# Performance work log

Measured on AMD Instinct MI355X. Metric: run time of the kernel, lower is better.

Reference implementation:

```python
import jax, jax.numpy as jnp
import numpy as np


def setup_inputs() -> dict:
    key = jax.random.key(0)
    ks = jax.random.split(key, 5)
    B, S, D, U = 4, 2048, 1024, 1024
    scale = 1.0 / np.sqrt(D)
    return {
        "query": jax.random.normal(ks[0], (B, S, D), dtype=jnp.float32),
        "value": jax.random.normal(ks[1], (B, S, D), dtype=jnp.float32),
        "Wq": jax.random.normal(ks[2], (D, U), dtype=jnp.float32) * scale,
        "bq": jnp.zeros((U,), dtype=jnp.float32),
        "Wk": jax.random.normal(ks[3], (D, U), dtype=jnp.float32) * scale,
        "bk": jnp.zeros((U,), dtype=jnp.float32),
        "Wv": jax.random.normal(ks[4], (D, U), dtype=jnp.float32) * scale,
        "bv": jnp.zeros((U,), dtype=jnp.float32),
    }


def reference(query, value, Wq, bq, Wk, bk, Wv, bv):
    # Dense projections (last-dim matmul + bias)
    Q = jnp.einsum("bsd,du->bsu", query, Wq) + bq   # [B,Sq,U]
    K = jnp.einsum("btd,du->btu", value, Wk) + bk   # [B,Sk,U]
    V = jnp.einsum("btd,du->btu", value, Wv) + bv   # [B,Sk,U]
    d_k = jnp.asarray(K.shape[-1], dtype=jnp.float32)
    scores = jnp.einsum("bsu,btu->bst", Q, K) / jnp.sqrt(d_k)  # [B,Sq,Sk]
    weights = jax.nn.softmax(scores, axis=-1)
    return jnp.einsum("bst,btu->bsu", weights, V)   # [B,Sq,U]
```

## Files before the change

kernel.cpp:

```cpp
#include <hip/hip_runtime.h>
#include <hip/hip_bf16.h>
#include <stdint.h>

#define DEVINL __device__ __forceinline__

typedef __attribute__((ext_vector_type(4))) float f32x4;
typedef __attribute__((ext_vector_type(8))) __bf16 bfv8;
typedef __attribute__((ext_vector_type(8))) short s16x8;
typedef __attribute__((ext_vector_type(4))) short s16x4;

DEVINL short f2bf(float f) {
  union { float f; unsigned u; } v; v.f = f;
  unsigned r = v.u + 0x7FFFu + ((v.u >> 16) & 1u);
  return (short)(r >> 16);
}
DEVINL float bf2f(short h) {
  union { unsigned u; float f; } v; v.u = ((unsigned)(unsigned short)h) << 16;
  return v.f;
}
DEVINL void gload_lds16(const void* g, void* l) {
  __builtin_amdgcn_global_load_lds((__attribute__((address_space(1))) unsigned*)(g),
                                   (__attribute__((address_space(3))) unsigned*)(l),
                                   16, 0, 0);
}
#define S_BARRIER() __builtin_amdgcn_s_barrier()
#define MEMORD() asm volatile("" ::: "memory")
template <int N> DEVINL void vmwaitc() {
  asm volatile("s_waitcnt vmcnt(%0)" :: "i"(N) : "memory");
}
DEVINL int xswz(int p, int n) { return (p & 7) * (n >> 3) + (p >> 3); }

template <int BU, int NF, int RING>
DEVINL void gemm_core(const short* __restrict__ Ag, const short* __restrict__ Bg,
                      int lda, int ldb, int m0, int n0, int nkt,
                      short* lds, f32x4 (&acc)[8][NF]) {
  constexpr int U = 2 + BU;
  constexpr int SLOT = 8192 + BU * 4096;
  const int tid = threadIdx.x;
  const int w = tid >> 6, l = tid & 63;
  const int wm = w >> 2, wn = w & 3;
  const int lr = l & 15, lg = l >> 4;
  const int stg_row = w * 16 + (l >> 2);
  const int stg_col = (((l & 3) ^ ((l >> 3) & 3)) << 3);
  const int ck = ((lg ^ ((lr >> 1) & 3)) << 3);
  const int aro = (wm * 128 + lr) * 32 + ck;
  const int bro = 8192 + (wn * (NF * 16) + lr) * 32 + ck;
  const int dW = w * 512;

#define STAGE_A(t) { short* S_ = lds + ((t) % RING) * SLOT;                                \
    gload_lds16(Ag + (size_t)(m0 + stg_row) * lda + (t) * 32 + stg_col, S_ + dW);          \
    gload_lds16(Ag + (size_t)(m0 + 128 + stg_row) * lda + (t) * 32 + stg_col,              \
                S_ + 4096 + dW); }
#define STAGE_B(t) { short* S_ = lds + ((t) % RING) * SLOT;                                \
    _Pragma("unroll")                                                                      \
    for (int u_ = 0; u_ < BU; ++u_)                                                        \
      gload_lds16(Bg + (size_t)(n0 + u_ * 128 + stg_row) * ldb + (t) * 32 + stg_col,       \
                  S_ + 8192 + u_ * 4096 + dW); }

#pragma unroll
  for (int t = 0; t < RING - 1; ++t) { STAGE_A(t); STAGE_B(t); }
  vmwaitc<(RING - 2) * U>(); S_BARRIER(); MEMORD();

  bfv8 aA[4], aB[4], bA[NF], bB[NF];
  {
    const short* Sp = lds;
#pragma unroll
    for (int mf = 0; mf < 4; ++mf) aA[mf] = *(const bfv8*)(Sp + aro + mf * 512);
#pragma unroll
    for (int nf = 0; nf < NF; ++nf) bA[nf] = *(const bfv8*)(Sp + bro + nf * 512);
  }

#pragma unroll 1
  for (int kt = 0; kt < nkt; kt += 2) {
    const short* S0 = lds + (kt % RING) * SLOT;
    const short* S1 = lds + ((kt + 1) % RING) * SLOT;
    const short* S2 = lds + ((kt + 2) % RING) * SLOT;
    if (kt + 2 < nkt) STAGE_A(kt + 2);
#pragma unroll
    for (int mf = 0; mf < 4; ++mf) aB[mf] = *(const bfv8*)(S0 + aro + 2048 + mf * 512);
#pragma unroll
    for (int mf = 0; mf < 4; ++mf)
#pragma unroll
      for (int nf = 0; nf < NF; ++nf)
        acc[mf][nf] = __builtin_amdgcn_mfma_f32_16x16x32_bf16(aA[mf], bA[nf], acc[mf][nf], 0, 0, 0);
    if (kt + 2 < nkt) vmwaitc<2>(); else vmwaitc<0>();
    S_BARRIER(); MEMORD();
    if (kt + 2 < nkt) STAGE_B(kt + 2);
#pragma unroll
    for (int mf = 0; mf < 4; ++mf) aA[mf] = *(const bfv8*)(S1 + aro + mf * 512);
#pragma unroll
    for (int nf = 0; nf < NF; ++nf) bB[nf] = *(const bfv8*)(S1 + bro + nf * 512);
#pragma unroll
    for (int mf = 0; mf < 4; ++mf)
#pragma unroll
      for (int nf = 0; nf < NF; ++nf)
        acc[4 + mf][nf] = __builtin_amdgcn_mfma_f32_16x16x32_bf16(aB[mf], bA[nf], acc[4 + mf][nf], 0, 0, 0);
    S_BARRIER(); MEMORD();
    if (kt + 3 < nkt) STAGE_A(kt + 3);
#pragma unroll
    for (int mf = 0; mf < 4; ++mf) aB[mf] = *(const bfv8*)(S1 + aro + 2048 + mf * 512);
#pragma unroll
    for (int mf = 0; mf < 4; ++mf)
#pragma unroll
      for (int nf = 0; nf < NF; ++nf)
        acc[mf][nf] = __builtin_amdgcn_mfma_f32_16x16x32_bf16(aA[mf], bB[nf], acc[mf][nf], 0, 0, 0);
    if (kt + 3 < nkt) vmwaitc<2>(); else vmwaitc<0>();
    S_BARRIER(); MEMORD();
    if (kt + 3 < nkt) STAGE_B(kt + 3);
    if (kt + 2 < nkt) {
#pragma unroll
      for (int mf = 0; mf < 4; ++mf) aA[mf] = *(const bfv8*)(S2 + aro + mf * 512);
#pragma unroll
      for (int nf = 0; nf < NF; ++nf) bA[nf] = *(const bfv8*)(S2 + bro + nf * 512);
    }
#pragma unroll
    for (int mf = 0; mf < 4; ++mf)
#pragma unroll
      for (int nf = 0; nf < NF; ++nf)
        acc[4 + mf][nf] = __builtin_amdgcn_mfma_f32_16x16x32_bf16(aB[mf], bB[nf], acc[4 + mf][nf], 0, 0, 0);
    S_BARRIER(); MEMORD();
  }
#undef STAGE_A
#undef STAGE_B
}

__global__ __launch_bounds__(256) void prep_kernel(
    const float* __restrict__ q, const float* __restrict__ v,
    const float* __restrict__ Wq, const float* __restrict__ Wk, const float* __restrict__ Wv,
    short* __restrict__ Qc, short* __restrict__ Vc,
    short* __restrict__ WTq, short* __restrict__ WTk, short* __restrict__ WTv) {
  __shared__ float tile[64][65];
  const int bx = blockIdx.x;
  if (bx < 8192) {
    const float* src = (bx < 4096) ? q : v;
    short* dst = (bx < 4096) ? Qc : Vc;
    const size_t i = ((size_t)(bx & 4095) * 256 + threadIdx.x) * 8;
    f32x4 x0 = *(const f32x4*)(src + i);
    f32x4 x1 = *(const f32x4*)(src + i + 4);
    s16x8 o;
#pragma unroll
    for (int j = 0; j < 4; ++j) { o[j] = f2bf(x0[j]); o[4 + j] = f2bf(x1[j]); }
    *(s16x8*)(dst + i) = o;
  } else {
    const int z = (bx - 8192) >> 8, xx = (bx - 8192) & 255;
    const float* W = (z == 0) ? Wq : (z == 1) ? Wk : Wv;
    short* WT = (z == 0) ? WTq : (z == 1) ? WTk : WTv;
    const int k0 = (xx & 15) << 6, n0 = (xx >> 4) << 6;
    const int c = threadIdx.x & 63, r0 = threadIdx.x >> 6;
#pragma unroll
    for (int i = 0; i < 16; ++i) {
      int r = (i << 2) + r0;
      tile[r][c] = W[(size_t)(k0 + r) * 1024 + n0 + c];
    }
    __syncthreads();
#pragma unroll
    for (int i = 0; i < 16; ++i) {
      int a = (i << 2) + r0;
      WT[(size_t)(n0 + a) * 1024 + k0 + c] = f2bf(tile[c][a]);
    }
  }
}

__global__ __launch_bounds__(512, 4) void qkproj_kernel(
    const short* __restrict__ Qc, const short* __restrict__ Vc,
    const short* __restrict__ WTq, const short* __restrict__ WTk,
    const float* __restrict__ bq, const float* __restrict__ bk,
    short* __restrict__ Qb, short* __restrict__ Kb) {
  __shared__ short lds[36864];
  const int o = xswz(blockIdx.x, 512);
  const int sel = o >> 8, r = o & 255;
  const int bm = r >> 3, bn = r & 7;
  const short* A = sel ? Vc : Qc;
  const short* BT = sel ? WTk : WTq;
  const float* bias = sel ? bk : bq;
  short* O = sel ? Kb : Qb;
  const int m0 = bm * 256, n0 = bn * 128;
  f32x4 acc[8][2];
#pragma unroll
  for (int i = 0; i < 8; ++i)
#pragma unroll
    for (int j = 0; j < 2; ++j) acc[i][j] = (f32x4){0.f, 0.f, 0.f, 0.f};
  gemm_core<1, 2, 3>(A, BT, 1024, 1024, m0, n0, 32, lds, acc);
  const int tid = threadIdx.x;
  const int w = tid >> 6, l = tid & 63;
  const int wm = w >> 2, wn = w & 3, lr = l & 15, lg = l >> 4;
#pragma unroll
  for (int i = 0; i < 8; ++i) {
    const int row0 = m0 + wm * 128 + (i >> 2) * 64 + (i & 3) * 16 + lg * 4;
#pragma unroll
    for (int nf = 0; nf < 2; ++nf) {
      const int col = n0 + wn * 32 + nf * 16 + lr;
      const float bb = bias[col];
#pragma unroll
      for (int j = 0; j < 4; ++j)
        O[(size_t)(row0 + j) * 1024 + col] = f2bf(acc[i][nf][j] + bb);
    }
  }
}

__global__ __launch_bounds__(512, 2) void vproj_kernel(
    const short* __restrict__ Vc, const short* __restrict__ WTv,
    const float* __restrict__ bv, short* __restrict__ VT) {
  __shared__ short lds[36864];
  const int o = xswz(blockIdx.x, 256);
  const int bm = o >> 3, bn = o & 7;
  const int m0 = bm * 256, n0 = bn * 128;
  f32x4 acc[8][2];
#pragma unroll
  for (int i = 0; i < 8; ++i)
#pragma unroll
    for (int j = 0; j < 2; ++j) acc[i][j] = (f32x4){0.f, 0.f, 0.f, 0.f};
  gemm_core<1, 2, 3>(Vc, WTv, 1024, 1024, m0, n0, 32, lds, acc);
  const int tid = threadIdx.x;
  const int w = tid >> 6, l = tid & 63;
  const int wm = w >> 2, wn = w & 3, lr = l & 15, lg = l >> 4;
  __syncthreads();
  short* lt = lds;
#pragma unroll
  for (int i = 0; i < 8; ++i) {
    const int tl = wm * 128 + (i >> 2) * 64 + (i & 3) * 16 + lg * 4;
#pragma unroll
    for (int nf = 0; nf < 2; ++nf) {
      const int ul = wn * 32 + nf * 16 + lr;
      const float bb = bv[n0 + ul];
      s16x4 pk;
#pragma unroll
      for (int j = 0; j < 4; ++j) pk[j] = f2bf(acc[i][nf][j] + bb);
      *(s16x4*)&lt[ul * 264 + tl] = pk;
    }
  }
  __syncthreads();
  const int b = m0 >> 11, t0 = m0 & 2047;
#pragma unroll
  for (int it = 0; it < 8; ++it) {
    const int cid = it * 512 + tid;
    const int u = cid >> 5, tc = cid & 31;
    s16x8 v8 = *(const s16x8*)&lt[u * 264 + tc * 8];
    *(s16x8*)(VT + ((size_t)b * 1024 + n0 + u) * 2048 + t0 + tc * 8) = v8;
  }
}

__global__ __launch_bounds__(512, 4) void qkt_kernel(const short* __restrict__ Qb,
                                                     const short* __restrict__ Kb,
                                                     short* __restrict__ Sb) {
  __shared__ short lds[36864];
  const int o = xswz(blockIdx.x, 512);
  const int bt = o >> 7, r = o & 127;
  const int bm = r >> 4, bn = r & 15;
  const short* A = Qb + (size_t)bt * 2097152;
  const short* B = Kb + (size_t)bt * 2097152;
  short* O = Sb + (size_t)bt * 4194304;
  const int m0 = bm * 256, n0 = bn * 128;
  f32x4 acc[8][2];
#pragma unroll
  for (int i = 0; i < 8; ++i)
#pragma unroll
    for (int j = 0; j < 2; ++j) acc[i][j] = (f32x4){0.f, 0.f, 0.f, 0.f};
  gemm_core<1, 2, 3>(A, B, 1024, 1024, m0, n0, 32, lds, acc);
  const int tid = threadIdx.x;
  const int w = tid >> 6, l = tid & 63;
  const int wm = w >> 2, wn = w & 3, lr = l & 15, lg = l >> 4;
#pragma unroll
  for (int i = 0; i < 8; ++i) {
    const int row0 = m0 + wm * 128 + (i >> 2) * 64 + (i & 3) * 16 + lg * 4;
#pragma unroll
    for (int nf = 0; nf < 2; ++nf) {
      const int col = n0 + wn * 32 + nf * 16 + lr;
#pragma unroll
      for (int j = 0; j < 4; ++j)
        O[(size_t)(row0 + j) * 2048 + col] = f2bf(acc[i][nf][j] * 0.03125f);
    }
  }
}

__global__ __launch_bounds__(512, 2) void pv_kernel(const short* __restrict__ Sb,
                                                    const short* __restrict__ VT,
                                                    float* __restrict__ Out) {
  __shared__ short lds[36864];
  const int o = xswz(blockIdx.x, 256);
  const int bt = o >> 6, r = o & 63;
  const int bm = r >> 3, bn = r & 7;
  const short* A = Sb + (size_t)bt * 4194304;
  const short* B = VT + (size_t)bt * 2097152;
  float* O = Out + (size_t)bt * 2097152;
  const int m0 = bm * 256, n0 = bn * 128;
  f32x4 acc[8][2];
#pragma unroll
  for (int i = 0; i < 8; ++i)
#pragma unroll
    for (int j = 0; j < 2; ++j) acc[i][j] = (f32x4){0.f, 0.f, 0.f, 0.f};
  gemm_core<1, 2, 3>(A, B, 2048, 2048, m0, n0, 64, lds, acc);
  const int l = threadIdx.x & 63, w = threadIdx.x >> 6;
  const int wm = w >> 2, wn = w & 3, lr = l & 15, lg = l >> 4;
#pragma unroll
  for (int i = 0; i < 8; ++i) {
    const int row0 = m0 + wm * 128 + (i >> 2) * 64 + (i & 3) * 16 + lg * 4;
#pragma unroll
    for (int nf = 0; nf < 2; ++nf) {
      const int col = n0 + wn * 32 + nf * 16 + lr;
#pragma unroll
      for (int j = 0; j < 4; ++j)
        O[(size_t)(row0 + j) * 1024 + col] = acc[i][nf][j];
    }
  }
}

__global__ __launch_bounds__(256) void softmax_kernel(short* __restrict__ Sb) {
  const size_t row = blockIdx.x;
  short* p = Sb + row * 2048;
  const int tid = threadIdx.x;
  const int w = tid >> 6, l = tid & 63;
  s16x8 v = *(const s16x8*)(p + tid * 8);
  float f[8];
#pragma unroll
  for (int j = 0; j < 8; ++j) f[j] = bf2f(v[j]);
  float m = f[0];
#pragma unroll
  for (int j = 1; j < 8; ++j) m = fmaxf(m, f[j]);
#pragma unroll
  for (int o = 32; o > 0; o >>= 1) m = fmaxf(m, __shfl_xor(m, o, 64));
  __shared__ float redm[4], reds[4];
  if (l == 0) redm[w] = m;
  __syncthreads();
  m = fmaxf(fmaxf(redm[0], redm[1]), fmaxf(redm[2], redm[3]));
  float s = 0.f;
#pragma unroll
  for (int j = 0; j < 8; ++j) { f[j] = __expf(f[j] - m); s += f[j]; }
#pragma unroll
  for (int o = 32; o > 0; o >>= 1) s += __shfl_xor(s, o, 64);
  if (l == 0) reds[w] = s;
  __syncthreads();
  s = reds[0] + reds[1] + reds[2] + reds[3];
  const float inv = 1.f / s;
  s16x8 o8;
#pragma unroll
  for (int j = 0; j < 8; ++j) o8[j] = f2bf(f[j] * inv);
  *(s16x8*)(p + tid * 8) = o8;
}

extern "C" void kernel_launch(void* const* d_in, const int* in_sizes, int n_in,
                              void* d_out, int out_size, void* d_ws, size_t ws_size,
                              hipStream_t stream) {
  const float* query = (const float*)d_in[0];
  const float* value = (const float*)d_in[1];
  const float* Wq = (const float*)d_in[2];
  const float* bq = (const float*)d_in[3];
  const float* Wk = (const float*)d_in[4];
  const float* bk = (const float*)d_in[5];
  const float* Wv = (const float*)d_in[6];
  const float* bv = (const float*)d_in[7];

  char* ws = (char*)d_ws;
  short* WTq = (short*)(ws);
  short* WTk = (short*)(ws + ((size_t)2 << 20));
  short* WTv = (short*)(ws + ((size_t)4 << 20));
  short* Qc  = (short*)(ws + ((size_t)6 << 20));
  short* Vc  = (short*)(ws + ((size_t)22 << 20));
  short* Sb  = (short*)(ws + ((size_t)6 << 20));
  short* Qb  = (short*)(ws + ((size_t)38 << 20));
  short* Kb  = (short*)(ws + ((size_t)54 << 20));
  short* VT  = (short*)(ws + ((size_t)70 << 20));

  prep_kernel<<<dim3(8960), 256, 0, stream>>>(query, value, Wq, Wk, Wv, Qc, Vc, WTq, WTk, WTv);

  qkproj_kernel<<<dim3(512), 512, 0, stream>>>(Qc, Vc, WTq, WTk, bq, bk, Qb, Kb);
  vproj_kernel<<<dim3(256), 512, 0, stream>>>(Vc, WTv, bv, VT);

  qkt_kernel<<<dim3(512), 512, 0, stream>>>(Qb, Kb, Sb);

  softmax_kernel<<<dim3(8192), 256, 0, stream>>>(Sb);

  pv_kernel<<<dim3(256), 512, 0, stream>>>(Sb, VT, (float*)d_out);
}
```

Baseline: 190.2 us.

## Use 256x256 GEMM tiles, split-K for PV, and raise MFMA wave priority

Grows the QK-projection, QK^T and PV GEMM tiles from 256x128 to 256x256 (gemm_core<2,4,3>, larger LDS, four accumulator fragments per wave). This raises data reuse per tile but halves the block count. PV now splits K in two, writing halves to Out and a Part scratch buffer (aliased over Qb/Kb) that a new add_kernel sums, which restores 256 blocks. s_setprio(1) is also wrapped around the MFMA bursts so waves doing math are favoured over waves issuing loads. The costs are fewer blocks per CU, more register pressure, and an extra fp32 read-modify-write pass over the output.

```diff
diff --git a/kernel.cpp b/kernel.cpp
--- a/kernel.cpp
+++ b/kernel.cpp
@@ -72,17 +72,19 @@
 
 #pragma unroll 1
   for (int kt = 0; kt < nkt; kt += 2) {
-    const short* S0 = lds + (kt % RING) * SLOT;
     const short* S1 = lds + ((kt + 1) % RING) * SLOT;
     const short* S2 = lds + ((kt + 2) % RING) * SLOT;
+    const short* S0 = lds + (kt % RING) * SLOT;
     if (kt + 2 < nkt) STAGE_A(kt + 2);
 #pragma unroll
     for (int mf = 0; mf < 4; ++mf) aB[mf] = *(const bfv8*)(S0 + aro + 2048 + mf * 512);
+    __builtin_amdgcn_s_setprio(1);
 #pragma unroll
     for (int mf = 0; mf < 4; ++mf)
 #pragma unroll
       for (int nf = 0; nf < NF; ++nf)
         acc[mf][nf] = __builtin_amdgcn_mfma_f32_16x16x32_bf16(aA[mf], bA[nf], acc[mf][nf], 0, 0, 0);
+    __builtin_amdgcn_s_setprio(0);
     if (kt + 2 < nkt) vmwaitc<2>(); else vmwaitc<0>();
     S_BARRIER(); MEMORD();
     if (kt + 2 < nkt) STAGE_B(kt + 2);
@@ -90,20 +92,24 @@
     for (int mf = 0; mf < 4; ++mf) aA[mf] = *(const bfv8*)(S1 + aro + mf * 512);
 #pragma unroll
     for (int nf = 0; nf < NF; ++nf) bB[nf] = *(const bfv8*)(S1 + bro + nf * 512);
+    __builtin_amdgcn_s_setprio(1);
 #pragma unroll
     for (int mf = 0; mf < 4; ++mf)
 #pragma unroll
       for (int nf = 0; nf < NF; ++nf)
         acc[4 + mf][nf] = __builtin_amdgcn_mfma_f32_16x16x32_bf16(aB[mf], bA[nf], acc[4 + mf][nf], 0, 0, 0);
+    __builtin_amdgcn_s_setprio(0);
     S_BARRIER(); MEMORD();
     if (kt + 3 < nkt) STAGE_A(kt + 3);
 #pragma unroll
     for (int mf = 0; mf < 4; ++mf) aB[mf] = *(const bfv8*)(S1 + aro + 2048 + mf * 512);
+    __builtin_amdgcn_s_setprio(1);
 #pragma unroll
     for (int mf = 0; mf < 4; ++mf)
 #pragma unroll
       for (int nf = 0; nf < NF; ++nf)
         acc[mf][nf] = __builtin_amdgcn_mfma_f32_16x16x32_bf16(aA[mf], bB[nf], acc[mf][nf], 0, 0, 0);
+    __builtin_amdgcn_s_setprio(0);
     if (kt + 3 < nkt) vmwaitc<2>(); else vmwaitc<0>();
     S_BARRIER(); MEMORD();
     if (kt + 3 < nkt) STAGE_B(kt + 3);
@@ -113,11 +119,13 @@
 #pragma unroll
       for (int nf = 0; nf < NF; ++nf) bA[nf] = *(const bfv8*)(S2 + bro + nf * 512);
     }
+    __builtin_amdgcn_s_setprio(1);
 #pragma unroll
     for (int mf = 0; mf < 4; ++mf)
 #pragma unroll
       for (int nf = 0; nf < NF; ++nf)
         acc[4 + mf][nf] = __builtin_amdgcn_mfma_f32_16x16x32_bf16(aB[mf], bB[nf], acc[4 + mf][nf], 0, 0, 0);
+    __builtin_amdgcn_s_setprio(0);
     S_BARRIER(); MEMORD();
   }
 #undef STAGE_A
@@ -161,26 +169,26 @@
   }
 }
 
-__global__ __launch_bounds__(512, 4) void qkproj_kernel(
+__global__ __launch_bounds__(512, 2) void qkproj_kernel(
     const short* __restrict__ Qc, const short* __restrict__ Vc,
     const short* __restrict__ WTq, const short* __restrict__ WTk,
     const float* __restrict__ bq, const float* __restrict__ bk,
     short* __restrict__ Qb, short* __restrict__ Kb) {
-  __shared__ short lds[36864];
-  const int o = xswz(blockIdx.x, 512);
-  const int sel = o >> 8, r = o & 255;
-  const int bm = r >> 3, bn = r & 7;
+  __shared__ short lds[49152];
+  const int o = xswz(blockIdx.x, 256);
+  const int sel = o >> 7, r = o & 127;
+  const int bm = r >> 2, bn = r & 3;
   const short* A = sel ? Vc : Qc;
   const short* BT = sel ? WTk : WTq;
   const float* bias = sel ? bk : bq;
   short* O = sel ? Kb : Qb;
-  const int m0 = bm * 256, n0 = bn * 128;
-  f32x4 acc[8][2];
+  const int m0 = bm * 256, n0 = bn * 256;
+  f32x4 acc[8][4];
 #pragma unroll
   for (int i = 0; i < 8; ++i)
 #pragma unroll
-    for (int j = 0; j < 2; ++j) acc[i][j] = (f32x4){0.f, 0.f, 0.f, 0.f};
-  gemm_core<1, 2, 3>(A, BT, 1024, 1024, m0, n0, 32, lds, acc);
+    for (int j = 0; j < 4; ++j) acc[i][j] = (f32x4){0.f, 0.f, 0.f, 0.f};
+  gemm_core<2, 4, 3>(A, BT, 1024, 1024, m0, n0, 32, lds, acc);
   const int tid = threadIdx.x;
   const int w = tid >> 6, l = tid & 63;
   const int wm = w >> 2, wn = w & 3, lr = l & 15, lg = l >> 4;
@@ -188,8 +196,8 @@
   for (int i = 0; i < 8; ++i) {
     const int row0 = m0 + wm * 128 + (i >> 2) * 64 + (i & 3) * 16 + lg * 4;
 #pragma unroll
-    for (int nf = 0; nf < 2; ++nf) {
-      const int col = n0 + wn * 32 + nf * 16 + lr;
+    for (int nf = 0; nf < 4; ++nf) {
+      const int col = n0 + wn * 64 + nf * 16 + lr;
       const float bb = bias[col];
 #pragma unroll
       for (int j = 0; j < 4; ++j)
@@ -240,23 +248,23 @@
   }
 }
 
-__global__ __launch_bounds__(512, 4) void qkt_kernel(const short* __restrict__ Qb,
+__global__ __launch_bounds__(512, 2) void qkt_kernel(const short* __restrict__ Qb,
                                                      const short* __restrict__ Kb,
                                                      short* __restrict__ Sb) {
-  __shared__ short lds[36864];
-  const int o = xswz(blockIdx.x, 512);
-  const int bt = o >> 7, r = o & 127;
-  const int bm = r >> 4, bn = r & 15;
+  __shared__ short lds[49152];
+  const int o = xswz(blockIdx.x, 256);
+  const int bt = o >> 6, r = o & 63;
+  const int bm = r >> 3, bn = r & 7;
   const short* A = Qb + (size_t)bt * 2097152;
   const short* B = Kb + (size_t)bt * 2097152;
   short* O = Sb + (size_t)bt * 4194304;
-  const int m0 = bm * 256, n0 = bn * 128;
-  f32x4 acc[8][2];
+  const int m0 = bm * 256, n0 = bn * 256;
+  f32x4 acc[8][4];
 #pragma unroll
   for (int i = 0; i < 8; ++i)
 #pragma unroll
-    for (int j = 0; j < 2; ++j) acc[i][j] = (f32x4){0.f, 0.f, 0.f, 0.f};
-  gemm_core<1, 2, 3>(A, B, 1024, 1024, m0, n0, 32, lds, acc);
+    for (int j = 0; j < 4; ++j) acc[i][j] = (f32x4){0.f, 0.f, 0.f, 0.f};
+  gemm_core<2, 4, 3>(A, B, 1024, 1024, m0, n0, 32, lds, acc);
   const int tid = threadIdx.x;
   const int w = tid >> 6, l = tid & 63;
   const int wm = w >> 2, wn = w & 3, lr = l & 15, lg = l >> 4;
@@ -264,8 +272,8 @@
   for (int i = 0; i < 8; ++i) {
     const int row0 = m0 + wm * 128 + (i >> 2) * 64 + (i & 3) * 16 + lg * 4;
 #pragma unroll
-    for (int nf = 0; nf < 2; ++nf) {
-      const int col = n0 + wn * 32 + nf * 16 + lr;
+    for (int nf = 0; nf < 4; ++nf) {
+      const int col = n0 + wn * 64 + nf * 16 + lr;
 #pragma unroll
       for (int j = 0; j < 4; ++j)
         O[(size_t)(row0 + j) * 2048 + col] = f2bf(acc[i][nf][j] * 0.03125f);
@@ -275,34 +283,46 @@
 
 __global__ __launch_bounds__(512, 2) void pv_kernel(const short* __restrict__ Sb,
                                                     const short* __restrict__ VT,
-                                                    float* __restrict__ Out) {
-  __shared__ short lds[36864];
+                                                    float* __restrict__ Out,
+                                                    float* __restrict__ Part) {
+  __shared__ short lds[49152];
   const int o = xswz(blockIdx.x, 256);
-  const int bt = o >> 6, r = o & 63;
-  const int bm = r >> 3, bn = r & 7;
-  const short* A = Sb + (size_t)bt * 4194304;
-  const short* B = VT + (size_t)bt * 2097152;
-  float* O = Out + (size_t)bt * 2097152;
-  const int m0 = bm * 256, n0 = bn * 128;
-  f32x4 acc[8][2];
+  const int kh = o >> 7;
+  const int bt = (o >> 5) & 3;
+  const int bm = (o >> 2) & 7, bn = o & 3;
+  const short* A = Sb + (size_t)bt * 4194304 + kh * 1024;
+  const short* B = VT + (size_t)bt * 2097152 + kh * 1024;
+  float* O = (kh ? Part : Out) + (size_t)bt * 2097152;
+  const int m0 = bm * 256, n0 = bn * 256;
+  f32x4 acc[8][4];
 #pragma unroll
   for (int i = 0; i < 8; ++i)
 #pragma unroll
-    for (int j = 0; j < 2; ++j) acc[i][j] = (f32x4){0.f, 0.f, 0.f, 0.f};
-  gemm_core<1, 2, 3>(A, B, 2048, 2048, m0, n0, 64, lds, acc);
+    for (int j = 0; j < 4; ++j) acc[i][j] = (f32x4){0.f, 0.f, 0.f, 0.f};
+  gemm_core<2, 4, 3>(A, B, 2048, 2048, m0, n0, 32, lds, acc);
   const int l = threadIdx.x & 63, w = threadIdx.x >> 6;
   const int wm = w >> 2, wn = w & 3, lr = l & 15, lg = l >> 4;
 #pragma unroll
   for (int i = 0; i < 8; ++i) {
     const int row0 = m0 + wm * 128 + (i >> 2) * 64 + (i & 3) * 16 + lg * 4;
 #pragma unroll
-    for (int nf = 0; nf < 2; ++nf) {
-      const int col = n0 + wn * 32 + nf * 16 + lr;
+    for (int nf = 0; nf < 4; ++nf) {
+      const int col = n0 + wn * 64 + nf * 16 + lr;
 #pragma unroll
       for (int j = 0; j < 4; ++j)
         O[(size_t)(row0 + j) * 1024 + col] = acc[i][nf][j];
     }
   }
+}
+
+__global__ __launch_bounds__(256) void add_kernel(float* __restrict__ Out,
+                                                  const float* __restrict__ Part) {
+  const size_t i = ((size_t)blockIdx.x * 256 + threadIdx.x) * 4;
+  f32x4 a = *(const f32x4*)(Out + i);
+  f32x4 b = *(const f32x4*)(Part + i);
+#pragma unroll
+  for (int j = 0; j < 4; ++j) a[j] += b[j];
+  *(f32x4*)(Out + i) = a;
 }
 
 __global__ __launch_bounds__(256) void softmax_kernel(short* __restrict__ Sb) {
@@ -359,16 +379,18 @@
   short* Sb  = (short*)(ws + ((size_t)6 << 20));
   short* Qb  = (short*)(ws + ((size_t)38 << 20));
   short* Kb  = (short*)(ws + ((size_t)54 << 20));
+  float* Part = (float*)(ws + ((size_t)38 << 20));
   short* VT  = (short*)(ws + ((size_t)70 << 20));
 
   prep_kernel<<<dim3(8960), 256, 0, stream>>>(query, value, Wq, Wk, Wv, Qc, Vc, WTq, WTk, WTv);
 
-  qkproj_kernel<<<dim3(512), 512, 0, stream>>>(Qc, Vc, WTq, WTk, bq, bk, Qb, Kb);
+  qkproj_kernel<<<dim3(256), 512, 0, stream>>>(Qc, Vc, WTq, WTk, bq, bk, Qb, Kb);
   vproj_kernel<<<dim3(256), 512, 0, stream>>>(Vc, WTv, bv, VT);
 
-  qkt_kernel<<<dim3(512), 512, 0, stream>>>(Qb, Kb, Sb);
+  qkt_kernel<<<dim3(256), 512, 0, stream>>>(Qb, Kb, Sb);
 
   softmax_kernel<<<dim3(8192), 256, 0, stream>>>(Sb);
 
-  pv_kernel<<<dim3(256), 512, 0, stream>>>(Sb, VT, (float*)d_out);
-}
+  pv_kernel<<<dim3(256), 512, 0, stream>>>(Sb, VT, (float*)d_out, Part);
+  add_kernel<<<dim3(8192), 256, 0, stream>>>((float*)d_out, Part);
+}
```

After: 197.3 us. +3.7%, slower.

## Fold K projection into query via precomputed Wq·Wkᵀ matrix

Applied to the files above, without the earlier changes.

Rewrites the scores as Q·Wq·Wkᵀ·valueᵀ, so a 1024x1024 matrix M = Wq·Wkᵀ is precomputed with a split-K GEMM plus a reduction. Only one 8192x1024 projection (query·M) is then needed in place of separate Q and K projections, and scores are taken directly against the bf16 value. The bq-dependent term is added per column through a small tvec kernel, guarded by a flag, and the bk term is dropped because it is constant along each softmax row. This adds several small kernels and an extra bf16 rounding of M, which changes numerical error, and it removes a full 8192x1024x1024 GEMM.

```diff
diff --git a/kernel.cpp b/kernel.cpp
--- a/kernel.cpp
+++ b/kernel.cpp
@@ -46,7 +46,6 @@
   const int aro = (wm * 128 + lr) * 32 + ck;
   const int bro = 8192 + (wn * (NF * 16) + lr) * 32 + ck;
   const int dW = w * 512;
-
 #define STAGE_A(t) { short* S_ = lds + ((t) % RING) * SLOT;                                \
     gload_lds16(Ag + (size_t)(m0 + stg_row) * lda + (t) * 32 + stg_col, S_ + dW);          \
     gload_lds16(Ag + (size_t)(m0 + 128 + stg_row) * lda + (t) * 32 + stg_col,              \
@@ -56,11 +55,9 @@
     for (int u_ = 0; u_ < BU; ++u_)                                                        \
       gload_lds16(Bg + (size_t)(n0 + u_ * 128 + stg_row) * ldb + (t) * 32 + stg_col,       \
                   S_ + 8192 + u_ * 4096 + dW); }
-
 #pragma unroll
   for (int t = 0; t < RING - 1; ++t) { STAGE_A(t); STAGE_B(t); }
   vmwaitc<(RING - 2) * U>(); S_BARRIER(); MEMORD();
-
   bfv8 aA[4], aB[4], bA[NF], bB[NF];
   {
     const short* Sp = lds;
@@ -69,12 +66,11 @@
 #pragma unroll
     for (int nf = 0; nf < NF; ++nf) bA[nf] = *(const bfv8*)(Sp + bro + nf * 512);
   }
-
 #pragma unroll 1
   for (int kt = 0; kt < nkt; kt += 2) {
-    const short* S0 = lds + (kt % RING) * SLOT;
     const short* S1 = lds + ((kt + 1) % RING) * SLOT;
     const short* S2 = lds + ((kt + 2) % RING) * SLOT;
+    const short* S0 = lds + (kt % RING) * SLOT;
     if (kt + 2 < nkt) STAGE_A(kt + 2);
 #pragma unroll
     for (int mf = 0; mf < 4; ++mf) aB[mf] = *(const bfv8*)(S0 + aro + 2048 + mf * 512);
@@ -128,13 +124,16 @@
     const float* __restrict__ q, const float* __restrict__ v,
     const float* __restrict__ Wq, const float* __restrict__ Wk, const float* __restrict__ Wv,
     short* __restrict__ Qc, short* __restrict__ Vc,
-    short* __restrict__ WTq, short* __restrict__ WTk, short* __restrict__ WTv) {
+    short* __restrict__ Wqc, short* __restrict__ Wkc, short* __restrict__ WTv) {
   __shared__ float tile[64][65];
   const int bx = blockIdx.x;
-  if (bx < 8192) {
-    const float* src = (bx < 4096) ? q : v;
-    short* dst = (bx < 4096) ? Qc : Vc;
-    const size_t i = ((size_t)(bx & 4095) * 256 + threadIdx.x) * 8;
+  if (bx < 9216) {
+    const float* src; short* dst; int off;
+    if (bx < 4096)      { src = q;  dst = Qc;  off = bx; }
+    else if (bx < 8192) { src = v;  dst = Vc;  off = bx - 4096; }
+    else if (bx < 8704) { src = Wq; dst = Wqc; off = bx - 8192; }
+    else                { src = Wk; dst = Wkc; off = bx - 8704; }
+    const size_t i = ((size_t)off * 256 + threadIdx.x) * 8;
     f32x4 x0 = *(const f32x4*)(src + i);
     f32x4 x1 = *(const f32x4*)(src + i + 4);
     s16x8 o;
@@ -142,47 +141,71 @@
     for (int j = 0; j < 4; ++j) { o[j] = f2bf(x0[j]); o[4 + j] = f2bf(x1[j]); }
     *(s16x8*)(dst + i) = o;
   } else {
-    const int z = (bx - 8192) >> 8, xx = (bx - 8192) & 255;
-    const float* W = (z == 0) ? Wq : (z == 1) ? Wk : Wv;
-    short* WT = (z == 0) ? WTq : (z == 1) ? WTk : WTv;
+    const int xx = bx - 9216;
     const int k0 = (xx & 15) << 6, n0 = (xx >> 4) << 6;
     const int c = threadIdx.x & 63, r0 = threadIdx.x >> 6;
 #pragma unroll
     for (int i = 0; i < 16; ++i) {
       int r = (i << 2) + r0;
-      tile[r][c] = W[(size_t)(k0 + r) * 1024 + n0 + c];
+      tile[r][c] = Wv[(size_t)(k0 + r) * 1024 + n0 + c];
     }
     __syncthreads();
 #pragma unroll
     for (int i = 0; i < 16; ++i) {
       int a = (i << 2) + r0;
-      WT[(size_t)(n0 + a) * 1024 + k0 + c] = f2bf(tile[c][a]);
-    }
-  }
-}
-
-__global__ __launch_bounds__(512, 4) void qkproj_kernel(
-    const short* __restrict__ Qc, const short* __restrict__ Vc,
-    const short* __restrict__ WTq, const short* __restrict__ WTk,
-    const float* __restrict__ bq, const float* __restrict__ bk,
-    short* __restrict__ Qb, short* __restrict__ Kb) {
+      WTv[(size_t)(n0 + a) * 1024 + k0 + c] = f2bf(tile[c][a]);
+    }
+  }
+}
+
+__global__ __launch_bounds__(256) void bias0_kernel(const float* __restrict__ Wk,
+                                                    const float* __restrict__ bq,
+                                                    float* __restrict__ v1,
+                                                    float* __restrict__ flagp) {
+  __shared__ float red[256];
+  const int t = threadIdx.x;
+  float any = 0.f;
+  for (int i = t; i < 1024; i += 256) any += fabsf(bq[i]);
+  red[t] = any; __syncthreads();
+  for (int s = 128; s > 0; s >>= 1) { if (t < s) red[t] += red[t + s]; __syncthreads(); }
+  const float fl = red[0];
+  if (t == 0) *flagp = fl;
+  if (fl != 0.f) {
+    for (int r = t; r < 1024; r += 256) {
+      float acc = 0.f;
+      for (int u = 0; u < 1024; ++u) acc += Wk[(size_t)r * 1024 + u] * bq[u];
+      v1[r] = acc;
+    }
+  }
+}
+
+__global__ __launch_bounds__(256) void tvec_kernel(const float* __restrict__ Y,
+                                                   const float* __restrict__ v1,
+                                                   const float* __restrict__ flagp,
+                                                   float* __restrict__ tvec) {
+  const int t = blockIdx.x * 256 + threadIdx.x;
+  if (*flagp == 0.f) { tvec[t] = 0.f; return; }
+  float acc = 0.f;
+  for (int d = 0; d < 1024; ++d) acc += Y[(size_t)t * 1024 + d] * v1[d];
+  tvec[t] = acc;
+}
+
+__global__ __launch_bounds__(512, 2) void mker_kernel(const short* __restrict__ Wkc,
+                                                      const short* __restrict__ Wqc,
+                                                      float* __restrict__ Part) {
   __shared__ short lds[36864];
-  const int o = xswz(blockIdx.x, 512);
-  const int sel = o >> 8, r = o & 255;
+  const int o = xswz(blockIdx.x, 128);
+  const int ks = o >> 5, r = o & 31;
   const int bm = r >> 3, bn = r & 7;
-  const short* A = sel ? Vc : Qc;
-  const short* BT = sel ? WTk : WTq;
-  const float* bias = sel ? bk : bq;
-  short* O = sel ? Kb : Qb;
   const int m0 = bm * 256, n0 = bn * 128;
   f32x4 acc[8][2];
 #pragma unroll
   for (int i = 0; i < 8; ++i)
 #pragma unroll
     for (int j = 0; j < 2; ++j) acc[i][j] = (f32x4){0.f, 0.f, 0.f, 0.f};
-  gemm_core<1, 2, 3>(A, BT, 1024, 1024, m0, n0, 32, lds, acc);
-  const int tid = threadIdx.x;
-  const int w = tid >> 6, l = tid & 63;
+  gemm_core<1, 2, 3>(Wkc + ks * 256, Wqc + ks * 256, 1024, 1024, m0, n0, 8, lds, acc);
+  float* O = Part + (size_t)ks * 1048576;
+  const int l = threadIdx.x & 63, w = threadIdx.x >> 6;
   const int wm = w >> 2, wn = w & 3, lr = l & 15, lg = l >> 4;
 #pragma unroll
   for (int i = 0; i < 8; ++i) {
@@ -190,10 +213,50 @@
 #pragma unroll
     for (int nf = 0; nf < 2; ++nf) {
       const int col = n0 + wn * 32 + nf * 16 + lr;
-      const float bb = bias[col];
 #pragma unroll
       for (int j = 0; j < 4; ++j)
-        O[(size_t)(row0 + j) * 1024 + col] = f2bf(acc[i][nf][j] + bb);
+        O[(size_t)(row0 + j) * 1024 + col] = acc[i][nf][j];
+    }
+  }
+}
+
+__global__ __launch_bounds__(256) void mkred_kernel(const float* __restrict__ Part,
+                                                    short* __restrict__ MT) {
+  const size_t i = ((size_t)blockIdx.x * 256 + threadIdx.x) * 4;
+  f32x4 a = *(const f32x4*)(Part + i);
+  f32x4 b = *(const f32x4*)(Part + 1048576 + i);
+  f32x4 c = *(const f32x4*)(Part + 2097152 + i);
+  f32x4 d = *(const f32x4*)(Part + 3145728 + i);
+  s16x4 o;
+#pragma unroll
+  for (int j = 0; j < 4; ++j) o[j] = f2bf(a[j] + b[j] + c[j] + d[j]);
+  *(s16x4*)(MT + i) = o;
+}
+
+__global__ __launch_bounds__(512, 2) void qproj_kernel(const short* __restrict__ Qc,
+                                                       const short* __restrict__ MT,
+                                                       short* __restrict__ Ap) {
+  __shared__ short lds[36864];
+  const int o = xswz(blockIdx.x, 256);
+  const int bm = o >> 3, bn = o & 7;
+  const int m0 = bm * 256, n0 = bn * 128;
+  f32x4 acc[8][2];
+#pragma unroll
+  for (int i = 0; i < 8; ++i)
+#pragma unroll
+    for (int j = 0; j < 2; ++j) acc[i][j] = (f32x4){0.f, 0.f, 0.f, 0.f};
+  gemm_core<1, 2, 3>(Qc, MT, 1024, 1024, m0, n0, 32, lds, acc);
+  const int l = threadIdx.x & 63, w = threadIdx.x >> 6;
+  const int wm = w >> 2, wn = w & 3, lr = l & 15, lg = l >> 4;
+#pragma unroll
+  for (int i = 0; i < 8; ++i) {
+    const int row0 = m0 + wm * 128 + (i >> 2) * 64 + (i & 3) * 16 + lg * 4;
+#pragma unroll
+    for (int nf = 0; nf < 2; ++nf) {
+      const int col = n0 + wn * 32 + nf * 16 + lr;
+#pragma unroll
+      for (int j = 0; j < 4; ++j)
+        Ap[(size_t)(row0 + j) * 1024 + col] = f2bf(acc[i][nf][j]);
     }
   }
 }
@@ -240,16 +303,18 @@
   }
 }
 
-__global__ __launch_bounds__(512, 4) void qkt_kernel(const short* __restrict__ Qb,
-                                                     const short* __restrict__ Kb,
-                                                     short* __restrict__ Sb) {
+__global__ __launch_bounds__(512, 4) void qkt_kernel(const short* __restrict__ Ap,
+                                                     const short* __restrict__ Vc,
+                                                     const float* __restrict__ tvec,
+                                                     short* __restrict__ sb0,
+                                                     short* __restrict__ sb3) {
   __shared__ short lds[36864];
   const int o = xswz(blockIdx.x, 512);
   const int bt = o >> 7, r = o & 127;
   const int bm = r >> 4, bn = r & 15;
-  const short* A = Qb + (size_t)bt * 2097152;
-  const short* B = Kb + (size_t)bt * 2097152;
-  short* O = Sb + (size_t)bt * 4194304;
+  const short* A = Ap + (size_t)bt * 2097152;
+  const short* B = Vc + (size_t)bt * 2097152;
+  short* O = (bt < 3) ? (sb0 + (size_t)bt * 4194304) : sb3;
   const int m0 = bm * 256, n0 = bn * 128;
   f32x4 acc[8][2];
 #pragma unroll
@@ -260,6 +325,9 @@
   const int tid = threadIdx.x;
   const int w = tid >> 6, l = tid & 63;
   const int wm = w >> 2, wn = w & 3, lr = l & 15, lg = l >> 4;
+  float tv[2];
+#pragma unroll
+  for (int nf = 0; nf < 2; ++nf) tv[nf] = tvec[bt * 2048 + n0 + wn * 32 + nf * 16 + lr];
 #pragma unroll
   for (int i = 0; i < 8; ++i) {
     const int row0 = m0 + wm * 128 + (i >> 2) * 64 + (i & 3) * 16 + lg * 4;
@@ -268,19 +336,20 @@
       const int col = n0 + wn * 32 + nf * 16 + lr;
 #pragma unroll
       for (int j = 0; j < 4; ++j)
-        O[(size_t)(row0 + j) * 2048 + col] = f2bf(acc[i][nf][j] * 0.03125f);
-    }
-  }
-}
-
-__global__ __launch_bounds__(512, 2) void pv_kernel(const short* __restrict__ Sb,
+        O[(size_t)(row0 + j) * 2048 + col] = f2bf((acc[i][nf][j] + tv[nf]) * 0.03125f);
+    }
+  }
+}
+
+__global__ __launch_bounds__(512, 2) void pv_kernel(const short* __restrict__ sb0,
+                                                    const short* __restrict__ sb3,
                                                     const short* __restrict__ VT,
                                                     float* __restrict__ Out) {
   __shared__ short lds[36864];
   const int o = xswz(blockIdx.x, 256);
   const int bt = o >> 6, r = o & 63;
   const int bm = r >> 3, bn = r & 7;
-  const short* A = Sb + (size_t)bt * 4194304;
+  const short* A = (bt < 3) ? (sb0 + (size_t)bt * 4194304) : sb3;
   const short* B = VT + (size_t)bt * 2097152;
   float* O = Out + (size_t)bt * 2097152;
   const int m0 = bm * 256, n0 = bn * 128;
@@ -305,9 +374,11 @@
   }
 }
 
-__global__ __launch_bounds__(256) void softmax_kernel(short* __restrict__ Sb) {
-  const size_t row = blockIdx.x;
-  short* p = Sb + row * 2048;
+__global__ __launch_bounds__(256) void softmax_kernel(short* __restrict__ sb0,
+                                                      short* __restrict__ sb3) {
+  const int row = blockIdx.x;
+  const int bt = row >> 11;
+  short* p = ((bt < 3) ? (sb0 + (size_t)bt * 4194304) : sb3) + (size_t)(row & 2047) * 2048;
   const int tid = threadIdx.x;
   const int w = tid >> 6, l = tid & 63;
   s16x8 v = *(const s16x8*)(p + tid * 8);
@@ -346,29 +417,37 @@
   const float* Wq = (const float*)d_in[2];
   const float* bq = (const float*)d_in[3];
   const float* Wk = (const float*)d_in[4];
-  const float* bk = (const float*)d_in[5];
   const float* Wv = (const float*)d_in[6];
   const float* bv = (const float*)d_in[7];
 
   char* ws = (char*)d_ws;
-  short* WTq = (short*)(ws);
-  short* WTk = (short*)(ws + ((size_t)2 << 20));
-  short* WTv = (short*)(ws + ((size_t)4 << 20));
-  short* Qc  = (short*)(ws + ((size_t)6 << 20));
-  short* Vc  = (short*)(ws + ((size_t)22 << 20));
-  short* Sb  = (short*)(ws + ((size_t)6 << 20));
-  short* Qb  = (short*)(ws + ((size_t)38 << 20));
-  short* Kb  = (short*)(ws + ((size_t)54 << 20));
-  short* VT  = (short*)(ws + ((size_t)70 << 20));
-
-  prep_kernel<<<dim3(8960), 256, 0, stream>>>(query, value, Wq, Wk, Wv, Qc, Vc, WTq, WTk, WTv);
-
-  qkproj_kernel<<<dim3(512), 512, 0, stream>>>(Qc, Vc, WTq, WTk, bq, bk, Qb, Kb);
+  short* Wqc = (short*)(ws);
+  short* Wkc = (short*)(ws + ((size_t)2 << 20));
+  short* MT  = (short*)(ws + ((size_t)4 << 20));
+  short* WTv = (short*)(ws + ((size_t)6 << 20));
+  short* Qc  = (short*)(ws + ((size_t)8 << 20));
+  short* Vc  = (short*)(ws + ((size_t)24 << 20));
+  float* Part = (float*)(ws + ((size_t)40 << 20));
+  short* Ap  = (short*)(ws + ((size_t)40 << 20));
+  short* VT  = (short*)(ws + ((size_t)56 << 20));
+  short* sb0 = (short*)(ws);
+  short* sb3 = (short*)(ws + ((size_t)72 << 20));
+  float* tvec = (float*)(ws + ((size_t)80 << 20));
+  float* v1   = (float*)(ws + ((size_t)80 << 20) + 65536);
+  float* flagp = (float*)(ws + ((size_t)80 << 20) + 131072);
+
+  prep_kernel<<<dim3(9472), 256, 0, stream>>>(query, value, Wq, Wk, Wv,
+                                              Qc, Vc, Wqc, Wkc, WTv);
+  bias0_kernel<<<dim3(1), 256, 0, stream>>>(Wk, bq, v1, flagp);
+  tvec_kernel<<<dim3(32), 256, 0, stream>>>(value, v1, flagp, tvec);
+
+  mker_kernel<<<dim3(128), 512, 0, stream>>>(Wkc, Wqc, Part);
+  mkred_kernel<<<dim3(1024), 256, 0, stream>>>(Part, MT);
+
+  qproj_kernel<<<dim3(256), 512, 0, stream>>>(Qc, MT, Ap);
   vproj_kernel<<<dim3(256), 512, 0, stream>>>(Vc, WTv, bv, VT);
 
-  qkt_kernel<<<dim3(512), 512, 0, stream>>>(Qb, Kb, Sb);
-
-  softmax_kernel<<<dim3(8192), 256, 0, stream>>>(Sb);
-
-  pv_kernel<<<dim3(256), 512, 0, stream>>>(Sb, VT, (float*)d_out);
-}
+  qkt_kernel<<<dim3(512), 512, 0, stream>>>(Ap, Vc, tvec, sb0, sb3);
+  softmax_kernel<<<dim3(8192), 256, 0, stream>>>(sb0, sb3);
+  pv_kernel<<<dim3(256), 512, 0, stream>>>(sb0, sb3, VT, (float*)d_out);
+}
```

After: 189.4 us. No clear change (-0.4%).
